# Performance work log

Hardware: AMD Instinct MI355X
Metric: run time of the kernel (lower is better)

Reference implementation:

```python
import jax, jax.numpy as jnp
import numpy as np

N, DIM, H = 4096, 768, 12
HD = DIM // H  # head_dim = 64


def setup_inputs() -> dict:
    key = jax.random.key(0)
    ks = jax.random.split(key, 7)
    std = 1.0 / np.sqrt(HD)
    return {
        "seq": jax.random.normal(ks[0], (N, DIM), dtype=jnp.float32),
        "Wq": jax.random.normal(ks[1], (H, HD, HD), dtype=jnp.float32) * std,
        "bq": jax.random.normal(ks[2], (H, HD), dtype=jnp.float32) * std,
        "Wk": jax.random.normal(ks[3], (H, HD, HD), dtype=jnp.float32) * std,
        "bk": jax.random.normal(ks[4], (H, HD), dtype=jnp.float32) * std,
        "Wv": jax.random.normal(ks[5], (H, HD, HD), dtype=jnp.float32) * std,
        "bv": jax.random.normal(ks[6], (H, HD), dtype=jnp.float32) * std,
    }


def reference(seq, Wq, bq, Wk, bk, Wv, bv):
    n = seq.shape[0]
    # split the feature dim into heads: [N, H, HD]
    s = seq.reshape(n, H, HD)
    # per-head linear projections (torch Linear: y = x W^T + b; W stored as [in,out])
    q = jnp.einsum("nhd,hde->hne", s, Wq) + bq[:, None, :]  # [H, N, HD]
    k = jnp.einsum("nhd,hde->hne", s, Wk) + bk[:, None, :]
    v = jnp.einsum("nhd,hde->hne", s, Wv) + bv[:, None, :]
    scale = 1.0 / jnp.sqrt(jnp.asarray(HD, dtype=seq.dtype))
    scores = jnp.einsum("hne,hme->hnm", q, k) * scale  # [H, N, N]
    attn = jax.nn.softmax(scores, axis=-1)
    out = jnp.einsum("hnm,hme->hne", attn, v)  # [H, N, HD]
    # hstack of per-head results == concat along features in head order
    return jnp.transpose(out, (1, 0, 2)).reshape(n, DIM)
```

## Files before the change

### kernel.cpp

```cpp
#include <hip/hip_runtime.h>
#include <stdint.h>
#include <stddef.h>

#define N   4096
#define DIM 768
#define H   12
#define HD  64

typedef __attribute__((ext_vector_type(4))) int   i32x4;
typedef __attribute__((ext_vector_type(4))) float f32x4;
typedef __attribute__((ext_vector_type(8))) short short8;

#define MFMA(acc, a, b) \
  acc = __builtin_amdgcn_mfma_f32_16x16x32_bf16(a, b, acc, 0, 0, 0)

static __device__ __forceinline__ float fast_exp2(float x) {
#if __has_builtin(__builtin_amdgcn_exp2f)
  return __builtin_amdgcn_exp2f(x);
#else
  return exp2f(x);
#endif
}

static __device__ __forceinline__ short to_bf16(float x) {
  union { float f; uint32_t u; } v; v.f = x;
  uint32_t u = v.u;
  u += 0x7fffu + ((u >> 16) & 1u);
  return (short)(u >> 16);
}

__global__ __launch_bounds__(256) void proj_kernel(
    const float* __restrict__ seq,
    const float* __restrict__ Wq, const float* __restrict__ bq,
    const float* __restrict__ Wk, const float* __restrict__ bk,
    const float* __restrict__ Wv, const float* __restrict__ bv,
    short* __restrict__ Qo, short* __restrict__ Ko, short* __restrict__ Vto)
{
  __shared__ float s_tile[64][64];
  __shared__ float w_lds[3][64][64];
  const int h  = blockIdx.y;
  const int r0 = blockIdx.x * 64;
  const int t  = (int)threadIdx.x;

#pragma unroll
  for (int i = 0; i < 16; ++i) {
    const int idx = t + i * 256;
    const int r = idx >> 6, c = idx & 63;
    s_tile[r][c]   = seq[(size_t)(r0 + r) * DIM + h * HD + c];
    w_lds[0][r][c] = Wq[h * 4096 + idx];
    w_lds[1][r][c] = Wk[h * 4096 + idx];
    w_lds[2][r][c] = Wv[h * 4096 + idx];
  }
  __syncthreads();

  const int w = t >> 6, l = t & 63;
  const int rb = w * 16;
  float aq[16], ak[16], av[16];
  const float bqv = bq[h * HD + l];
  const float bkv = bk[h * HD + l];
  const float bvv = bv[h * HD + l];
#pragma unroll
  for (int r = 0; r < 16; ++r) { aq[r] = bqv; ak[r] = bkv; av[r] = bvv; }

#pragma unroll 4
  for (int d = 0; d < 64; ++d) {
    const float wq = w_lds[0][d][l];
    const float wk = w_lds[1][d][l];
    const float wv = w_lds[2][d][l];
#pragma unroll
    for (int r = 0; r < 16; ++r) {
      const float sv = s_tile[rb + r][d];
      aq[r] = fmaf(sv, wq, aq[r]);
      ak[r] = fmaf(sv, wk, ak[r]);
      av[r] = fmaf(sv, wv, av[r]);
    }
  }

  const float QSC = 0.1803368801111204f;
#pragma unroll
  for (int r = 0; r < 16; ++r) {
    const int n = r0 + rb + r;
    Qo[((size_t)h * N + n) * HD + l] = to_bf16(aq[r] * QSC);
    Ko[((size_t)h * N + n) * HD + l] = to_bf16(ak[r]);
    const int loc = n & 63;
    const int ns  = (n & ~63) | ((loc & 0x1C) << 1) | ((loc & 32) >> 3) | (loc & 3);
    Vto[((size_t)h * HD + l) * N + ns] = to_bf16(av[r]);
  }
}

__global__ __launch_bounds__(256) void attn_kernel(
    const short* __restrict__ Q, const short* __restrict__ K,
    const short* __restrict__ Vt, float* __restrict__ out)
{
  __shared__ __align__(16) char lds[32768];

  const int h  = blockIdx.y;
  const int q0 = blockIdx.x * 64;
  const int t  = (int)threadIdx.x;
  const int w  = t >> 6, l = t & 63, lr = l & 15, lg = l >> 4;

  const short* __restrict__ Qw = Q + ((size_t)h * N + q0 + w * 16) * HD;
  const char*  __restrict__ Kb = (const char*)(K  + (size_t)h * N * HD);
  const char*  __restrict__ Vb = (const char*)(Vt + (size_t)h * HD * N);

  short8 qf[2];
#pragma unroll
  for (int ds = 0; ds < 2; ++ds)
    qf[ds] = *(const short8*)(Qw + lr * HD + ds * 32 + lg * 8);

  f32x4 o[4], o5;
  o5 = f32x4{0.f, 0.f, 0.f, 0.f};
#pragma unroll
  for (int eb = 0; eb < 4; ++eb) o[eb] = f32x4{0.f, 0.f, 0.f, 0.f};
  const short8 vones = {0x3F80, 0x3F80, 0x3F80, 0x3F80,
                        0x3F80, 0x3F80, 0x3F80, 0x3F80};

  const int c0   = w * 2;
  const int c1   = c0 + 1;
  const int sr0  = c0 * 8 + (l >> 3);
  const int sr1  = sr0 + 8;
  const int scol = ((l & 7) * 16) ^ ((l >> 3) << 4);
  const int kdo0 = c0 * 1024 + l * 16;
  const int kdo1 = c1 * 1024 + l * 16;
  const char* const ks0 = Kb + (size_t)sr0 * 128 + scol;
  const char* const ks1 = Kb + (size_t)sr1 * 128 + scol;
  const char* const vs0 = Vb + (size_t)sr0 * (N * 2) + scol;
  const char* const vs1 = Vb + (size_t)sr1 * (N * 2) + scol;

  i32x4 rk0 = *(const i32x4*)ks0;
  i32x4 rk1 = *(const i32x4*)ks1;
  i32x4 rv0 = *(const i32x4*)vs0;
  i32x4 rv1 = *(const i32x4*)vs1;
  *(i32x4*)(lds + kdo0)        = rk0;
  *(i32x4*)(lds + kdo1)        = rk1;
  *(i32x4*)(lds + 8192 + kdo0) = rv0;
  *(i32x4*)(lds + 8192 + kdo1) = rv1;
  __syncthreads();

  for (int it = 0; it < N / 64; ++it) {
    const int  j1 = (it + 1) * 64;
    const bool pf = j1 < N;
    if (pf) {
      rk0 = *(const i32x4*)(ks0 + (size_t)j1 * 128);
      rk1 = *(const i32x4*)(ks1 + (size_t)j1 * 128);
      rv0 = *(const i32x4*)(vs0 + (size_t)j1 * 2);
      rv1 = *(const i32x4*)(vs1 + (size_t)j1 * 2);
    }
    const char* k_lds = lds + (it & 1) * 16384;
    const char* v_lds = k_lds + 8192;

    f32x4 s[4];
#pragma unroll
    for (int kb = 0; kb < 4; ++kb) {
      const int krow = kb * 16 + lr;
      const int kswz = (krow & 7) << 4;
      const char* kr = k_lds + krow * 128;
      const short8 kf0 = *(const short8*)(kr + ((lg * 16) ^ kswz));
      const short8 kf1 = *(const short8*)(kr + ((64 + lg * 16) ^ kswz));
      f32x4 acc = {0.f, 0.f, 0.f, 0.f};
      MFMA(acc, kf0, qf[0]);
      MFMA(acc, kf1, qf[1]);
      s[kb] = acc;
    }

#pragma unroll
    for (int kb = 0; kb < 4; ++kb)
#pragma unroll
      for (int r = 0; r < 4; ++r)
        s[kb][r] = fast_exp2(s[kb][r]);

    short8 pa0, pa1;
#pragma unroll
    for (int r = 0; r < 4; ++r) {
      pa0[r]     = to_bf16(s[0][r]);
      pa0[4 + r] = to_bf16(s[2][r]);
      pa1[r]     = to_bf16(s[1][r]);
      pa1[4 + r] = to_bf16(s[3][r]);
    }

    MFMA(o5, pa0, vones);
    MFMA(o5, pa1, vones);
#pragma unroll
    for (int eb = 0; eb < 4; ++eb) {
      const int vrow = eb * 16 + lr;
      const int vswz = (vrow & 7) << 4;
      const char* vr = v_lds + vrow * 128;
      const short8 vf0 = *(const short8*)(vr + ((lg * 16) ^ vswz));
      const short8 vf1 = *(const short8*)(vr + ((64 + lg * 16) ^ vswz));
      MFMA(o[eb], pa0, vf0);
      MFMA(o[eb], pa1, vf1);
    }

    if (pf) {
      char* const kn = lds + ((it + 1) & 1) * 16384;
      *(i32x4*)(kn + kdo0)        = rk0;
      *(i32x4*)(kn + kdo1)        = rk1;
      *(i32x4*)(kn + 8192 + kdo0) = rv0;
      *(i32x4*)(kn + 8192 + kdo1) = rv1;
    }
    __syncthreads();
  }

#pragma unroll
  for (int r = 0; r < 4; ++r) {
    const float inv = 1.0f / o5[r];
    const int n = q0 + w * 16 + lg * 4 + r;
    float* orow = out + (size_t)n * DIM + h * HD;
#pragma unroll
    for (int eb = 0; eb < 4; ++eb)
      orow[eb * 16 + lr] = o[eb][r] * inv;
  }
}

extern "C" void kernel_launch(void* const* d_in, const int* in_sizes, int n_in,
                              void* d_out, int out_size, void* d_ws, size_t ws_size,
                              hipStream_t stream) {
  const float* seq = (const float*)d_in[0];
  const float* Wq  = (const float*)d_in[1];
  const float* bq  = (const float*)d_in[2];
  const float* Wk  = (const float*)d_in[3];
  const float* bk  = (const float*)d_in[4];
  const float* Wv  = (const float*)d_in[5];
  const float* bv  = (const float*)d_in[6];
  float* out = (float*)d_out;

  short* Qw  = (short*)d_ws;
  short* Kw  = Qw + (size_t)H * N * HD;
  short* Vtw = Kw + (size_t)H * N * HD;

  proj_kernel<<<dim3(N / 64, H), 256, 0, stream>>>(seq, Wq, bq, Wk, bk, Wv, bv,
                                                   Qw, Kw, Vtw);
  attn_kernel<<<dim3(N / 64, H), 256, 0, stream>>>(Qw, Kw, Vtw, out);
}
```

Baseline: 116.2 us.

## Use direct global-to-LDS loads, cheaper bf16 packing, transposed seq tile in proj

The attention kernel's K/V tile staging now uses global_load_lds, which writes straight into the double-buffered LDS instead of going through registers and an explicit LDS store at the end of the loop. The P-matrix bf16 conversion moves from per-element round-to-nearest-even to a round-half-up add plus a single perm that packs two values. In the projection kernel the seq tile is stored transposed with padding so each thread reads its 16 rows with vector LDS loads. Risks: global_load_lds with 16-byte width needs gfx950 support and the right per-lane addressing, since the LDS destination is implicitly based on the lane id and may not match kdo offsets. The bf16 rounding also changes slightly on ties.

Result: faster. 108.3 us (-6.8%).

```diff
diff --git a/kernel.cpp b/kernel.cpp
--- a/kernel.cpp
+++ b/kernel.cpp
@@ -13,6 +13,11 @@
 
 #define MFMA(acc, a, b) \
   acc = __builtin_amdgcn_mfma_f32_16x16x32_bf16(a, b, acc, 0, 0, 0)
+
+#define GLOAD_LDS(gsrc, ldst) \
+  __builtin_amdgcn_global_load_lds( \
+      (const __attribute__((address_space(1))) uint32_t*)(gsrc), \
+      (__attribute__((address_space(3))) uint32_t*)(ldst), 16, 0, 0)
 
 static __device__ __forceinline__ float fast_exp2(float x) {
 #if __has_builtin(__builtin_amdgcn_exp2f)
@@ -20,6 +25,12 @@
 #else
   return exp2f(x);
 #endif
+}
+
+static __device__ __forceinline__ int pack_bf16(float lo, float hi) {
+  const uint32_t ulo = __builtin_bit_cast(uint32_t, lo) + 0x8000u;
+  const uint32_t uhi = __builtin_bit_cast(uint32_t, hi) + 0x8000u;
+  return (int)__builtin_amdgcn_perm(uhi, ulo, 0x07060302u);
 }
 
 static __device__ __forceinline__ short to_bf16(float x) {
@@ -36,7 +47,7 @@
     const float* __restrict__ Wv, const float* __restrict__ bv,
     short* __restrict__ Qo, short* __restrict__ Ko, short* __restrict__ Vto)
 {
-  __shared__ float s_tile[64][64];
+  __shared__ float sT[64][68];
   __shared__ float w_lds[3][64][64];
   const int h  = blockIdx.y;
   const int r0 = blockIdx.x * 64;
@@ -46,7 +57,7 @@
   for (int i = 0; i < 16; ++i) {
     const int idx = t + i * 256;
     const int r = idx >> 6, c = idx & 63;
-    s_tile[r][c]   = seq[(size_t)(r0 + r) * DIM + h * HD + c];
+    sT[c][r]       = seq[(size_t)(r0 + r) * DIM + h * HD + c];
     w_lds[0][r][c] = Wq[h * 4096 + idx];
     w_lds[1][r][c] = Wk[h * 4096 + idx];
     w_lds[2][r][c] = Wv[h * 4096 + idx];
@@ -67,12 +78,22 @@
     const float wq = w_lds[0][d][l];
     const float wk = w_lds[1][d][l];
     const float wv = w_lds[2][d][l];
-#pragma unroll
-    for (int r = 0; r < 16; ++r) {
-      const float sv = s_tile[rb + r][d];
-      aq[r] = fmaf(sv, wq, aq[r]);
-      ak[r] = fmaf(sv, wk, ak[r]);
-      av[r] = fmaf(sv, wv, av[r]);
+    const f32x4* sp = (const f32x4*)&sT[d][rb];
+    const f32x4 s0 = sp[0], s1 = sp[1], s2 = sp[2], s3 = sp[3];
+#pragma unroll
+    for (int r = 0; r < 4; ++r) {
+      aq[r]      = fmaf(s0[r], wq, aq[r]);
+      ak[r]      = fmaf(s0[r], wk, ak[r]);
+      av[r]      = fmaf(s0[r], wv, av[r]);
+      aq[4 + r]  = fmaf(s1[r], wq, aq[4 + r]);
+      ak[4 + r]  = fmaf(s1[r], wk, ak[4 + r]);
+      av[4 + r]  = fmaf(s1[r], wv, av[4 + r]);
+      aq[8 + r]  = fmaf(s2[r], wq, aq[8 + r]);
+      ak[8 + r]  = fmaf(s2[r], wk, ak[8 + r]);
+      av[8 + r]  = fmaf(s2[r], wv, av[8 + r]);
+      aq[12 + r] = fmaf(s3[r], wq, aq[12 + r]);
+      ak[12 + r] = fmaf(s3[r], wk, ak[12 + r]);
+      av[12 + r] = fmaf(s3[r], wv, av[12 + r]);
     }
   }
 
@@ -127,24 +148,21 @@
   const char* const vs0 = Vb + (size_t)sr0 * (N * 2) + scol;
   const char* const vs1 = Vb + (size_t)sr1 * (N * 2) + scol;
 
-  i32x4 rk0 = *(const i32x4*)ks0;
-  i32x4 rk1 = *(const i32x4*)ks1;
-  i32x4 rv0 = *(const i32x4*)vs0;
-  i32x4 rv1 = *(const i32x4*)vs1;
-  *(i32x4*)(lds + kdo0)        = rk0;
-  *(i32x4*)(lds + kdo1)        = rk1;
-  *(i32x4*)(lds + 8192 + kdo0) = rv0;
-  *(i32x4*)(lds + 8192 + kdo1) = rv1;
+  GLOAD_LDS(ks0, lds + kdo0);
+  GLOAD_LDS(ks1, lds + kdo1);
+  GLOAD_LDS(vs0, lds + 8192 + kdo0);
+  GLOAD_LDS(vs1, lds + 8192 + kdo1);
   __syncthreads();
 
   for (int it = 0; it < N / 64; ++it) {
     const int  j1 = (it + 1) * 64;
     const bool pf = j1 < N;
     if (pf) {
-      rk0 = *(const i32x4*)(ks0 + (size_t)j1 * 128);
-      rk1 = *(const i32x4*)(ks1 + (size_t)j1 * 128);
-      rv0 = *(const i32x4*)(vs0 + (size_t)j1 * 2);
-      rv1 = *(const i32x4*)(vs1 + (size_t)j1 * 2);
+      char* const nb = lds + ((it + 1) & 1) * 16384;
+      GLOAD_LDS(ks0 + (size_t)j1 * 128, nb + kdo0);
+      GLOAD_LDS(ks1 + (size_t)j1 * 128, nb + kdo1);
+      GLOAD_LDS(vs0 + (size_t)j1 * 2,   nb + 8192 + kdo0);
+      GLOAD_LDS(vs1 + (size_t)j1 * 2,   nb + 8192 + kdo1);
     }
     const char* k_lds = lds + (it & 1) * 16384;
     const char* v_lds = k_lds + 8192;
@@ -169,14 +187,17 @@
       for (int r = 0; r < 4; ++r)
         s[kb][r] = fast_exp2(s[kb][r]);
 
-    short8 pa0, pa1;
-#pragma unroll
-    for (int r = 0; r < 4; ++r) {
-      pa0[r]     = to_bf16(s[0][r]);
-      pa0[4 + r] = to_bf16(s[2][r]);
-      pa1[r]     = to_bf16(s[1][r]);
-      pa1[4 + r] = to_bf16(s[3][r]);
-    }
+    i32x4 p0, p1;
+    p0[0] = pack_bf16(s[0][0], s[0][1]);
+    p0[1] = pack_bf16(s[0][2], s[0][3]);
+    p0[2] = pack_bf16(s[2][0], s[2][1]);
+    p0[3] = pack_bf16(s[2][2], s[2][3]);
+    p1[0] = pack_bf16(s[1][0], s[1][1]);
+    p1[1] = pack_bf16(s[1][2], s[1][3]);
+    p1[2] = pack_bf16(s[3][0], s[3][1]);
+    p1[3] = pack_bf16(s[3][2], s[3][3]);
+    const short8 pa0 = __builtin_bit_cast(short8, p0);
+    const short8 pa1 = __builtin_bit_cast(short8, p1);
 
     MFMA(o5, pa0, vones);
     MFMA(o5, pa1, vones);
@@ -191,13 +212,6 @@
       MFMA(o[eb], pa1, vf1);
     }
 
-    if (pf) {
-      char* const kn = lds + ((it + 1) & 1) * 16384;
-      *(i32x4*)(kn + kdo0)        = rk0;
-      *(i32x4*)(kn + kdo1)        = rk1;
-      *(i32x4*)(kn + 8192 + kdo0) = rv0;
-      *(i32x4*)(kn + 8192 + kdo1) = rv1;
-    }
     __syncthreads();
   }
 
```
